# Kernel tuning notes

Hardware: AMD Instinct MI355X
Metric: run time of the kernel (lower is better)

## Reference

```python
import jax, jax.numpy as jnp
import numpy as np

B, L = 32, 200
NUM_C, NUM_D, DIM_V = 256, 32, 128


def setup_inputs() -> dict:
    key = jax.random.key(0)
    ks = jax.random.split(key, 20)
    def n(k, shape, s=0.05):
        return (jax.random.normal(k, shape) * s).astype(jnp.float32)
    return {
        "c_seq": jax.random.randint(ks[0], (B, L), 0, NUM_C),
        "d_seq": jax.random.randint(ks[1], (B, L), 0, NUM_D),
        "r_seq": jax.random.uniform(ks[2], (B, L), dtype=jnp.float32),
        # learned params
        "X": n(ks[3], (NUM_C * NUM_D, DIM_V), 0.1),      # Embedding table
        "v_r": n(ks[4], (DIM_V,), 0.1),
        "v_beta": n(ks[5], (DIM_V,), 0.1),
        # GRU (torch layout: gates [r|z|n] stacked)
        "W_ih": n(ks[6], (3 * DIM_V, 2 * DIM_V)),
        "W_hh": n(ks[7], (3 * DIM_V, DIM_V)),
        "b_ih": n(ks[8], (3 * DIM_V,)),
        "b_hh": n(ks[9], (3 * DIM_V,)),
        # linear_1: dim_v -> dim_v -> num_d (dropout = identity in eval)
        "W1a": n(ks[10], (DIM_V, DIM_V)), "b1a": n(ks[11], (DIM_V,)),
        "W1b": n(ks[12], (NUM_D, DIM_V)), "b1b": n(ks[13], (NUM_D,)),
        # linear_2: 3*dim_v -> dim_v -> num_d
        "W2a": n(ks[14], (DIM_V, 3 * DIM_V)), "b2a": n(ks[15], (DIM_V,)),
        "W2b": n(ks[16], (NUM_D, DIM_V)), "b2b": n(ks[17], (NUM_D,)),
    }


def reference(c_seq, d_seq, r_seq, X, v_r, v_beta, W_ih, W_hh, b_ih, b_hh,
              W1a, b1a, W1b, b1b, W2a, b2a, W2b, b2b):
    # embedding lookup: x = c + num_c * d
    v_x_seq = X[c_seq + NUM_C * d_seq]              # [B,L,V]
    v_r_seq = r_seq[..., None] * v_r                # [B,L,V]
    gru_in = jnp.concatenate([v_x_seq, v_r_seq], -1)  # [B,L,2V]

    # GRU (torch semantics), precompute input projections
    gx = jnp.einsum('blf,gf->blg', gru_in, W_ih) + b_ih  # [B,L,3V]

    def gru_step(h, gx_t):
        gh = h @ W_hh.T + b_hh
        xr, xz, xn = jnp.split(gx_t, 3, axis=-1)
        hr, hz, hn = jnp.split(gh, 3, axis=-1)
        r = jax.nn.sigmoid(xr + hr)
        z = jax.nn.sigmoid(xz + hz)
        n_ = jnp.tanh(xn + r * hn)
        h = (1.0 - z) * n_ + z * h
        return h, h

    h0 = jnp.zeros((B, DIM_V), dtype=gru_in.dtype)
    _, h_seq = jax.lax.scan(gru_step, h0, jnp.swapaxes(gx, 0, 1))
    h_seq = jnp.swapaxes(h_seq, 0, 1)               # [B,L,V]

    # linear_1 (dropout is identity at inference)
    alpha_seq = jax.nn.relu(h_seq @ W1a.T + b1a) @ W1b.T + b1b  # [B,L,num_d]

    # sequential memory update; one-hot gather/scatter expressed as true
    # gather C[b, c_t, d_t] and row scatter C[b, c_t, :] = new_c (same math)
    bidx = jnp.arange(B)

    def mem_step(C, inp):
        c_t, d_t, vx_t, vr_t = inp
        beta = C[bidx, c_t, d_t]                    # [B]
        v_beta_t = beta[:, None] * v_beta           # [B,V]
        zcat = jnp.concatenate([v_beta_t, vx_t, vr_t], -1)  # [B,3V]
        new_c = jax.nn.relu(zcat @ W2a.T + b2a) @ W2b.T + b2b  # [B,num_d]
        C = C.at[bidx, c_t].set(new_c)
        return C, C

    C0 = jnp.zeros((B, NUM_C, NUM_D), jnp.float32)
    _, C_seq = jax.lax.scan(
        mem_step, C0,
        (jnp.swapaxes(c_seq, 0, 1), jnp.swapaxes(d_seq, 0, 1),
         jnp.swapaxes(v_x_seq, 0, 1), jnp.swapaxes(v_r_seq, 0, 1)))
    C_seq = jnp.swapaxes(C_seq, 0, 1)               # [B,L,num_c,num_d]
    return alpha_seq, h_seq, C_seq
```

## Files before the change

kernel.cpp:

```cpp
#include <hip/hip_runtime.h>
#include <hip/hip_bf16.h>

typedef unsigned short u16;
typedef unsigned int u32;
typedef short short8 __attribute__((ext_vector_type(8)));
typedef float f32x4 __attribute__((ext_vector_type(4)));

constexpr int BATCH = 32, L = 200, NUM_C = 256, NUM_D = 32, V = 128;
constexpr int G3 = 384;
constexpr int KQ = 512;
constexpr int ROWS = BATCH * L;
constexpr int TP = 208;
constexpr size_t ALPHA_OFF = 0;
constexpr size_t H_OFF = (size_t)ROWS * NUM_D;
constexpr size_t C_OFF = H_OFF + (size_t)ROWS * V;

__device__ int g_gcnt;
__device__ int g_cflag[32];

__device__ inline u16 f2bf(float f) {
  __hip_bfloat16 h = __float2bfloat16(f);
  return __builtin_bit_cast(u16, h);
}
__device__ inline float bf2f(u16 u) { u32 x = ((u32)u) << 16; return __builtin_bit_cast(float, x); }

__device__ inline void cvt32(const float* __restrict__ src, u16* __restrict__ dst) {
#pragma unroll
  for (int j0 = 0; j0 < 32; j0 += 4) {
    const f32x4 v = *(const f32x4*)(src + j0);
    ushort4 s;
    s.x = f2bf(v[0]); s.y = f2bf(v[1]); s.z = f2bf(v[2]); s.w = f2bf(v[3]);
    *(ushort4*)(dst + j0) = s;
  }
}
__device__ inline short8 ldfrag(const float* __restrict__ p) {
  const f32x4 a = *(const f32x4*)p, b = *(const f32x4*)(p + 4);
  short8 s;
  s[0] = (short)f2bf(a[0]); s[1] = (short)f2bf(a[1]);
  s[2] = (short)f2bf(a[2]); s[3] = (short)f2bf(a[3]);
  s[4] = (short)f2bf(b[0]); s[5] = (short)f2bf(b[1]);
  s[6] = (short)f2bf(b[2]); s[7] = (short)f2bf(b[3]);
  return s;
}

__global__ __launch_bounds__(256) void k1(
    const int* __restrict__ c_seq, const int* __restrict__ d_seq,
    const float* __restrict__ r_seq, const float* __restrict__ X,
    const float* __restrict__ v_r, const float* __restrict__ W_ih,
    const float* __restrict__ W2a, const float* __restrict__ b_ih,
    const float* __restrict__ b2a, float* __restrict__ Qout)
{
  __shared__ __align__(16) u16 Als[64][144];
  __shared__ __align__(16) u16 Bls[64][144];
  const int tid = threadIdx.x;
  if (blockIdx.x == 0 && blockIdx.y == 0 && tid == 0) {
    g_gcnt = 0;
#pragma unroll
    for (int i = 0; i < 32; ++i) g_cflag[i] = 0;
  }
  const int mt = blockIdx.x, nt = blockIdx.y;
  const int lane = tid & 63, w = tid >> 6;
  const int q = lane >> 4, m = lane & 15;

  f32x4 acc[4];
#pragma unroll
  for (int i = 0; i < 4; ++i) acc[i] = (f32x4)0.0f;

  const int r0 = tid >> 2;
  const int kc = (tid & 3) * 32;
  const int rowg = mt * 64 + r0;
  const int gcolB = nt * 64 + r0;

  for (int s = 0; s < 2; ++s) {
    if (s) __syncthreads();
    if (s == 0) {
      const int idx = c_seq[rowg] + NUM_C * d_seq[rowg];
      cvt32(X + (size_t)idx * V + kc, &Als[r0][kc]);
    } else {
      const float rv = r_seq[rowg];
#pragma unroll
      for (int j0 = 0; j0 < 32; j0 += 4) {
        const f32x4 v = *(const f32x4*)(v_r + kc + j0);
        ushort4 sv;
        sv.x = f2bf(rv * v[0]); sv.y = f2bf(rv * v[1]);
        sv.z = f2bf(rv * v[2]); sv.w = f2bf(rv * v[3]);
        *(ushort4*)&Als[r0][kc + j0] = sv;
      }
    }
    {
      const float* src = (gcolB < G3)
        ? (W_ih + (size_t)gcolB * 256 + s * 128 + kc)
        : (W2a + (size_t)(gcolB - G3) * G3 + V + s * 128 + kc);
      cvt32(src, &Bls[r0][kc]);
    }
    __syncthreads();
#pragma unroll
    for (int c = 0; c < 4; ++c) {
      const short8 af = *(const short8*)&Als[w * 16 + m][32 * c + 8 * q];
#pragma unroll
      for (int i = 0; i < 4; ++i) {
        const short8 bf = *(const short8*)&Bls[i * 16 + m][32 * c + 8 * q];
        acc[i] = __builtin_amdgcn_mfma_f32_16x16x32_bf16(af, bf, acc[i], 0, 0, 0);
      }
    }
  }
#pragma unroll
  for (int i = 0; i < 4; ++i) {
    const int col = nt * 64 + i * 16 + m;
    const float bias = (col < G3) ? b_ih[col] : b2a[col - G3];
#pragma unroll
    for (int r = 0; r < 4; ++r) {
      const int rowo = mt * 64 + w * 16 + q * 4 + r;
      Qout[(size_t)rowo * KQ + col] = acc[i][r] + bias;
    }
  }
}

union ShK23 {
  struct { u16 h_bf[2][V]; } g;
  struct {
    int cb[TP]; int db[TP]; int sp[TP];
    float nr[TP][36];
    float u[V];
    int maxd;
  } s;
  struct { int cb[L]; float stage[L][NUM_D]; } f;
  struct { u16 hls[64][144]; u16 hid[64][144]; } a;
  struct { char p[84000]; } pad;
};

__global__ __launch_bounds__(256, 1) void k23(
    const int* __restrict__ c_seq, const int* __restrict__ d_seq,
    const float* __restrict__ W_hh, const float* __restrict__ b_hh,
    const float* __restrict__ W2a, const float* __restrict__ v_beta,
    const float* __restrict__ W2b, const float* __restrict__ b2b,
    const float* __restrict__ W1a, const float* __restrict__ b1a,
    const float* __restrict__ W1b, const float* __restrict__ b1b,
    const float* __restrict__ Q, float* __restrict__ out)
{
  __shared__ __align__(16) ShK23 sh;
  const int tid = threadIdx.x;
  const int l = tid & 63, w = tid >> 6, q = l >> 4, m = l & 15;
  const int blk = blockIdx.x;

  if (blk < 32) {
    const int b = blk;
    if (tid < V) sh.g.h_bf[0][tid] = 0;
    __syncthreads();
    short8 wf[6][4];
    float bhh[6]; int gcol[6];
#pragma unroll
    for (int i = 0; i < 6; ++i) {
      const int g = (w + 4 * i) * 16 + m;
      gcol[i] = g;
      bhh[i] = b_hh[g];
#pragma unroll
      for (int c = 0; c < 4; ++c)
        wf[i][c] = ldfrag(W_hh + (size_t)g * V + 32 * c + 8 * q);
    }
    const float* Qb = Q + (size_t)b * L * KQ;
    float* outh = out + H_OFF + (size_t)b * L * V;
    const int vi0 = 16 * w + m, vi1 = 64 + 16 * w + m;
    float hold[2] = {0.f, 0.f};
    float hst[2] = {0.f, 0.f};
    const f32x4 z4 = (f32x4)0.0f;
    float gxA[6], gxB[6];
#pragma unroll
    for (int i = 0; i < 6; ++i) gxA[i] = Qb[gcol[i]];
#pragma unroll
    for (int i = 0; i < 6; ++i) gxB[i] = Qb[KQ + gcol[i]];

    auto step = [&](int t, float (&gx)[6]) {
      const int rs = t & 1, wsl = rs ^ 1;
      short8 af[4];
#pragma unroll
      for (int c = 0; c < 4; ++c)
        af[c] = *(const short8*)&sh.g.h_bf[rs][32 * c + 8 * q];
      if (t > 0 && q == 0) {
        outh[(size_t)(t - 1) * V + vi0] = hst[0];
        outh[(size_t)(t - 1) * V + vi1] = hst[1];
      }
      f32x4 acc[6];
#pragma unroll
      for (int i = 0; i < 6; ++i)
        acc[i] = __builtin_amdgcn_mfma_f32_16x16x32_bf16(af[0], wf[i][0], z4, 0, 0, 0);
#pragma unroll
      for (int c = 1; c < 4; ++c)
#pragma unroll
        for (int i = 0; i < 6; ++i)
          acc[i] = __builtin_amdgcn_mfma_f32_16x16x32_bf16(af[c], wf[i][c], acc[i], 0, 0, 0);
      float hnew[2];
#pragma unroll
      for (int s = 0; s < 2; ++s) {
        const float xr = gx[0 + s] + acc[0 + s][0] + bhh[0 + s];
        const float xz = gx[2 + s] + acc[2 + s][0] + bhh[2 + s];
        const float ghn = acc[4 + s][0] + bhh[4 + s];
        const float r = 1.f / (1.f + __expf(-xr));
        const float z = 1.f / (1.f + __expf(-xz));
        const float xn = gx[4 + s] + r * ghn;
        const float e = __expf(2.f * xn);
        const float n = 1.f - 2.f / (e + 1.f);
        hnew[s] = (1.f - z) * n + z * hold[s];
      }
      if (q == 0) {
        sh.g.h_bf[wsl][vi0] = f2bf(hnew[0]);
        sh.g.h_bf[wsl][vi1] = f2bf(hnew[1]);
      }
      hold[0] = hnew[0]; hold[1] = hnew[1];
      hst[0] = hnew[0]; hst[1] = hnew[1];
      if (t + 2 < L) {
        const float* Qr = Qb + (size_t)(t + 2) * KQ;
#pragma unroll
        for (int i = 0; i < 6; ++i) gx[i] = Qr[gcol[i]];
      }
      __builtin_amdgcn_s_waitcnt(0xc07f);
      __builtin_amdgcn_s_barrier();
    };

    for (int t = 0; t < L; t += 2) {
      step(t, gxA);
      step(t + 1, gxB);
    }
    if (q == 0) {
      outh[(size_t)(L - 1) * V + vi0] = hst[0];
      outh[(size_t)(L - 1) * V + vi1] = hst[1];
    }
    __threadfence();
    __syncthreads();
    if (tid == 0) atomicAdd(&g_gcnt, 1);
  } else if (blk < 64) {
    const int b = blk - 32;
    for (int i = tid; i < TP; i += 256) {
      int c = -1, d = 0;
      if (i < L) { c = c_seq[b * L + i]; d = d_seq[b * L + i]; }
      sh.s.cb[i] = c; sh.s.db[i] = d; sh.s.sp[i] = -1;
    }
    if (tid < V) {
      float a = 0.f;
      const float* wr = W2a + (size_t)tid * G3;
      for (int k = 0; k < V; ++k) a += wr[k] * v_beta[k];
      sh.s.u[tid] = a;
    }
    if (tid == 0) sh.s.maxd = 0;
    __syncthreads();
    {
      const int c = tid;
      int prev = -1;
      for (int t4 = 0; t4 < L; t4 += 4) {
        const int4 v = *(const int4*)&sh.s.cb[t4];
        if (v.x == c) { sh.s.sp[t4 + 0] = prev; prev = t4 + 0; }
        if (v.y == c) { sh.s.sp[t4 + 1] = prev; prev = t4 + 1; }
        if (v.z == c) { sh.s.sp[t4 + 2] = prev; prev = t4 + 2; }
        if (v.w == c) { sh.s.sp[t4 + 3] = prev; prev = t4 + 3; }
      }
    }
    __syncthreads();
    {
      int dmx = 0;
      for (int t = tid; t < L; t += 256) {
        int dd = 0, s = sh.s.sp[t];
        while (s >= 0) { ++dd; s = sh.s.sp[s]; }
        dmx = dmx > dd ? dmx : dd;
      }
      atomicMax(&sh.s.maxd, dmx);
    }
    __syncthreads();
    const int rounds = sh.s.maxd + 1;
    float ureg[4][8];
#pragma unroll
    for (int c = 0; c < 4; ++c)
#pragma unroll
      for (int j = 0; j < 8; ++j) ureg[c][j] = sh.s.u[32 * c + 8 * q + j];
    short8 wbf[2][4];
    float bb[2];
#pragma unroll
    for (int tt = 0; tt < 2; ++tt) {
#pragma unroll
      for (int c = 0; c < 4; ++c)
        wbf[tt][c] = ldfrag(W2b + (size_t)(tt * 16 + m) * V + 32 * c + 8 * q);
      bb[tt] = b2b[tt * 16 + m];
    }
    const f32x4 z4 = (f32x4)0.0f;
    for (int rd = 0; rd < rounds; ++rd) {
      for (int ti = w; ti < 13; ti += 4) {
        const int t0 = ti * 16;
        const int tt = t0 + m;
        const bool ok = tt < L;
        const int spv = ok ? sh.s.sp[tt] : -1;
        const int dbv = ok ? sh.s.db[tt] : 0;
        const float beta = (spv >= 0) ? sh.s.nr[spv][dbv] : 0.f;
        const float* pr = Q + ((size_t)b * L + tt) * KQ + G3 + 8 * q;
        short8 af[4];
#pragma unroll
        for (int c = 0; c < 4; ++c) {
          const f32x4 p0 = ok ? *(const f32x4*)(pr + 32 * c) : (f32x4)0.0f;
          const f32x4 p1 = ok ? *(const f32x4*)(pr + 32 * c + 4) : (f32x4)0.0f;
          short8 a;
#pragma unroll
          for (int j = 0; j < 8; ++j) {
            const float pv = (j < 4) ? p0[j] : p1[j - 4];
            a[j] = (short)f2bf(fmaxf(beta * ureg[c][j] + pv, 0.f));
          }
          af[c] = a;
        }
        f32x4 a0 = z4, a1 = z4;
#pragma unroll
        for (int c = 0; c < 4; ++c) {
          a0 = __builtin_amdgcn_mfma_f32_16x16x32_bf16(af[c], wbf[0][c], a0, 0, 0, 0);
          a1 = __builtin_amdgcn_mfma_f32_16x16x32_bf16(af[c], wbf[1][c], a1, 0, 0, 0);
        }
#pragma unroll
        for (int r = 0; r < 4; ++r) {
          const int tr = t0 + q * 4 + r;
          sh.s.nr[tr][m]      = a0[r] + bb[0];
          sh.s.nr[tr][16 + m] = a1[r] + bb[1];
        }
      }
      __syncthreads();
    }
    float* outc = out + C_OFF + (size_t)b * L * (NUM_C * NUM_D);
    const int j4 = (tid & 7) * 4;
    for (int t = tid >> 3; t < L; t += 32) {
      const int c = sh.s.cb[t];
      float* oc = outc + (size_t)t * (NUM_C * NUM_D) + c * NUM_D + j4;
      *(f32x4*)oc = *(const f32x4*)&sh.s.nr[t][j4];
    }
    __threadfence();
    __syncthreads();
    if (tid == 0) atomicExch(&g_cflag[b], 1);
  } else if (blk < 192) {
    const int blk2 = blk - 64;
    const int b = blk2 >> 2, cbase = (blk2 & 3) * 64;
    if (tid < L) sh.f.cb[tid] = c_seq[b * L + tid];
    if (tid == 0) {
      while (atomicAdd(&g_cflag[b], 0) == 0) __builtin_amdgcn_s_sleep(32);
    }
    __syncthreads();
    __threadfence();
    if (tid < L) {
      const int c = sh.f.cb[tid];
      if (c >= cbase && c < cbase + 64) {
        const float* src = out + C_OFF + ((size_t)b * L + tid) * (NUM_C * NUM_D) + (size_t)c * NUM_D;
#pragma unroll
        for (int j = 0; j < 8; ++j)
          *(f32x4*)&sh.f.stage[tid][j * 4] = *(const f32x4*)(src + j * 4);
      }
    }
    __syncthreads();
    const int cl = tid >> 2, dq = (tid & 3) * 8;
    const int myc = cbase + cl;
    float* base = out + C_OFF + (size_t)b * L * (NUM_C * NUM_D) + (size_t)myc * NUM_D + dq;
    f32x4 cur0 = (f32x4)0.0f, cur1 = (f32x4)0.0f;
    for (int t = 0; t < L; ++t) {
      if (sh.f.cb[t] == myc) {
        cur0 = *(const f32x4*)&sh.f.stage[t][dq];
        cur1 = *(const f32x4*)&sh.f.stage[t][dq + 4];
      }
      *(f32x4*)base = cur0;
      *(f32x4*)(base + 4) = cur1;
      base += NUM_C * NUM_D;
    }
  } else {
    const int ab0 = (blk - 192) * 2;
    if (tid == 0) {
      while (atomicAdd(&g_gcnt, 0) < 32) __builtin_amdgcn_s_sleep(32);
    }
    __syncthreads();
    __threadfence();
    for (int sub = 0; sub < 2; ++sub) {
      const int ab = ab0 + sub;
      __syncthreads();
      {
        const int r0 = tid >> 2, kc = (tid & 3) * 32;
        cvt32(out + H_OFF + (size_t)(ab * 64 + r0) * V + kc, &sh.a.hls[r0][kc]);
      }
      __syncthreads();
      f32x4 acc1[8];
#pragma unroll
      for (int i = 0; i < 8; ++i) acc1[i] = (f32x4)0.0f;
#pragma unroll
      for (int c = 0; c < 4; ++c) {
        const short8 af = *(const short8*)&sh.a.hls[w * 16 + m][32 * c + 8 * q];
#pragma unroll
        for (int i = 0; i < 8; ++i) {
          const short8 bf = ldfrag(W1a + (size_t)(i * 16 + m) * V + 32 * c + 8 * q);
          acc1[i] = __builtin_amdgcn_mfma_f32_16x16x32_bf16(af, bf, acc1[i], 0, 0, 0);
        }
      }
#pragma unroll
      for (int i = 0; i < 8; ++i) {
        const int col = i * 16 + m;
        const float bias = b1a[col];
#pragma unroll
        for (int r = 0; r < 4; ++r)
          sh.a.hid[w * 16 + q * 4 + r][col] = f2bf(fmaxf(acc1[i][r] + bias, 0.f));
      }
      __syncthreads();
      f32x4 acc2[2];
      acc2[0] = (f32x4)0.0f; acc2[1] = (f32x4)0.0f;
#pragma unroll
      for (int c = 0; c < 4; ++c) {
        const short8 af = *(const short8*)&sh.a.hid[w * 16 + m][32 * c + 8 * q];
#pragma unroll
        for (int tt = 0; tt < 2; ++tt) {
          const short8 bf = ldfrag(W1b + (size_t)(tt * 16 + m) * V + 32 * c + 8 * q);
          acc2[tt] = __builtin_amdgcn_mfma_f32_16x16x32_bf16(af, bf, acc2[tt], 0, 0, 0);
        }
      }
#pragma unroll
      for (int tt = 0; tt < 2; ++tt) {
        const int col = tt * 16 + m;
        const float bias = b1b[col];
#pragma unroll
        for (int r = 0; r < 4; ++r) {
          const int row = ab * 64 + w * 16 + q * 4 + r;
          out[ALPHA_OFF + (size_t)row * NUM_D + col] = acc2[tt][r] + bias;
        }
      }
    }
  }
}

extern "C" void kernel_launch(void* const* d_in, const int* in_sizes, int n_in,
                              void* d_out, int out_size, void* d_ws, size_t ws_size,
                              hipStream_t stream) {
  const int*   c_seq  = (const int*)d_in[0];
  const int*   d_seq  = (const int*)d_in[1];
  const float* r_seq  = (const float*)d_in[2];
  const float* X      = (const float*)d_in[3];
  const float* v_r    = (const float*)d_in[4];
  const float* v_beta = (const float*)d_in[5];
  const float* W_ih   = (const float*)d_in[6];
  const float* W_hh   = (const float*)d_in[7];
  const float* b_ih   = (const float*)d_in[8];
  const float* b_hh   = (const float*)d_in[9];
  const float* W1a    = (const float*)d_in[10];
  const float* b1a    = (const float*)d_in[11];
  const float* W1b    = (const float*)d_in[12];
  const float* b1b    = (const float*)d_in[13];
  const float* W2a    = (const float*)d_in[14];
  const float* b2a    = (const float*)d_in[15];
  const float* W2b    = (const float*)d_in[16];
  const float* b2b    = (const float*)d_in[17];
  float* out = (float*)d_out;
  float* Q = (float*)d_ws;

  k1<<<dim3(100, 8), 256, 0, stream>>>(c_seq, d_seq, r_seq, X, v_r, W_ih, W2a, b_ih, b2a, Q);
  k23<<<242, 256, 0, stream>>>(c_seq, d_seq, W_hh, b_hh, W2a, v_beta, W2b, b2b,
                               W1a, b1a, W1b, b1b, Q, out);
}
```

Measured before the change: 381.4 us.

## Overlap alpha MLP with GRU by signalling per-50-step chunk completion

The GRU blocks now publish progress after every 50 timesteps through four chunk counters instead of a single completion counter. The alpha-MLP blocks process (chunk, tile) jobs and wait only for the chunk they need, so linear_1 runs alongside the remaining recurrence instead of after all of it. This adds periodic fences and block barriers inside the GRU loop, and remaps rows so each 64-row tile draws from the per-batch time slices of one chunk.

```diff
diff --git a/kernel.cpp b/kernel.cpp
--- a/kernel.cpp
+++ b/kernel.cpp
@@ -11,11 +11,12 @@
 constexpr int KQ = 512;
 constexpr int ROWS = BATCH * L;
 constexpr int TP = 208;
+constexpr int TCH = 50;
 constexpr size_t ALPHA_OFF = 0;
 constexpr size_t H_OFF = (size_t)ROWS * NUM_D;
 constexpr size_t C_OFF = H_OFF + (size_t)ROWS * V;
 
-__device__ int g_gcnt;
+__device__ int g_hcnt[4];
 __device__ int g_cflag[32];
 
 __device__ inline u16 f2bf(float f) {
@@ -54,7 +55,8 @@
   __shared__ __align__(16) u16 Bls[64][144];
   const int tid = threadIdx.x;
   if (blockIdx.x == 0 && blockIdx.y == 0 && tid == 0) {
-    g_gcnt = 0;
+#pragma unroll
+    for (int i = 0; i < 4; ++i) g_hcnt[i] = 0;
 #pragma unroll
     for (int i = 0; i < 32; ++i) g_cflag[i] = 0;
   }
@@ -215,6 +217,12 @@
       }
       __builtin_amdgcn_s_waitcnt(0xc07f);
       __builtin_amdgcn_s_barrier();
+      if (t > 0 && t % TCH == 0) {
+        __builtin_amdgcn_s_waitcnt(0x0f70);
+        __syncthreads();
+        __threadfence();
+        if (tid == 0) atomicAdd(&g_hcnt[t / TCH - 1], 1);
+      }
     };
 
     for (int t = 0; t < L; t += 2) {
@@ -225,9 +233,10 @@
       outh[(size_t)(L - 1) * V + vi0] = hst[0];
       outh[(size_t)(L - 1) * V + vi1] = hst[1];
     }
+    __builtin_amdgcn_s_waitcnt(0x0f70);
+    __syncthreads();
     __threadfence();
-    __syncthreads();
-    if (tid == 0) atomicAdd(&g_gcnt, 1);
+    if (tid == 0) atomicAdd(&g_hcnt[3], 1);
   } else if (blk < 64) {
     const int b = blk - 32;
     for (int i = tid; i < TP; i += 256) {
@@ -361,18 +370,20 @@
       base += NUM_C * NUM_D;
     }
   } else {
-    const int ab0 = (blk - 192) * 2;
-    if (tid == 0) {
-      while (atomicAdd(&g_gcnt, 0) < 32) __builtin_amdgcn_s_sleep(32);
-    }
-    __syncthreads();
-    __threadfence();
-    for (int sub = 0; sub < 2; ++sub) {
-      const int ab = ab0 + sub;
+    for (int jj = 0; jj < 2; ++jj) {
+      const int job = (blk - 192) * 2 + jj;
+      const int ck = job / 25, tile = job % 25;
+      if (tid == 0) {
+        while (atomicAdd(&g_hcnt[ck], 0) < 32) __builtin_amdgcn_s_sleep(32);
+      }
       __syncthreads();
+      __threadfence();
       {
         const int r0 = tid >> 2, kc = (tid & 3) * 32;
-        cvt32(out + H_OFF + (size_t)(ab * 64 + r0) * V + kc, &sh.a.hls[r0][kc]);
+        const int idx = tile * 64 + r0;
+        const int bb = idx / TCH, ss = idx % TCH;
+        const int row = bb * L + ck * TCH + ss;
+        cvt32(out + H_OFF + (size_t)row * V + kc, &sh.a.hls[r0][kc]);
       }
       __syncthreads();
       f32x4 acc1[8];
@@ -413,10 +424,13 @@
         const float bias = b1b[col];
 #pragma unroll
         for (int r = 0; r < 4; ++r) {
-          const int row = ab * 64 + w * 16 + q * 4 + r;
+          const int idx = tile * 64 + w * 16 + q * 4 + r;
+          const int bb = idx / TCH, ss = idx % TCH;
+          const int row = bb * L + ck * TCH + ss;
           out[ALPHA_OFF + (size_t)row * NUM_D + col] = acc2[tt][r] + bias;
         }
       }
+      __syncthreads();
     }
   }
 }
```

New measurement: 413.8 us. 1.09x slower.
